# Performance work log

Measured on AMD Instinct MI355X. Metric: run time of the kernel, lower is better.

## Reference

```python
import jax, jax.numpy as jnp
import numpy as np

HEADS = 8
DIM_HEAD = 64
DIM = 512
SCALE = DIM ** -0.5  # NOTE: original scales by dim**-0.5, not dim_head**-0.5


def setup_inputs() -> dict:
    key = jax.random.key(0)
    k1, k2, k3 = jax.random.split(key, 3)
    b, n = 2, 4096
    x = jax.random.normal(k1, (b, n, DIM), dtype=jnp.float32)
    Wqkv = jax.random.normal(k2, (DIM, 3 * HEADS * DIM_HEAD), dtype=jnp.float32) * (DIM ** -0.5)
    Wout = jax.random.normal(k3, (HEADS * DIM_HEAD, DIM), dtype=jnp.float32) * ((HEADS * DIM_HEAD) ** -0.5)
    b_out = jnp.zeros((DIM,), dtype=jnp.float32)
    return {"x": x, "Wqkv": Wqkv, "Wout": Wout, "b_out": b_out}


def reference(x, Wqkv, Wout, b_out):
    b, n, _ = x.shape
    h, d = HEADS, DIM_HEAD
    qkv = x @ Wqkv  # [b, n, 3*h*d]
    q, k, v = jnp.split(qkv, 3, axis=-1)
    to_heads = lambda t: t.reshape(b, n, h, d).transpose(0, 2, 1, 3)  # [b,h,n,d]
    q, k, v = to_heads(q), to_heads(k), to_heads(v)
    half = n // 2
    q_s, q_t = q[:, :, :half], q[:, :, half:]
    k_t = k[:, :, half:]  # k_s is unused in the original module
    v_s, v_t = v[:, :, :half], v[:, :, half:]
    # temporal branch: q_t attends to k_t, reads v_t
    dots_t = jnp.einsum('bhid,bhjd->bhij', q_t, k_t) * SCALE
    # spatial branch: cross-term q_s attends to k_t, reads v_s
    dots_s = jnp.einsum('bhid,bhjd->bhij', q_s, k_t) * SCALE
    attn_s = jax.nn.softmax(dots_s, axis=-1)
    attn_t = jax.nn.softmax(dots_t, axis=-1)
    out_s = jnp.einsum('bhij,bhjd->bhid', attn_s, v_s)
    out_t = jnp.einsum('bhij,bhjd->bhid', attn_t, v_t)
    out = jnp.concatenate([out_s, out_t], axis=2)  # [b,h,n,d]
    out = out.transpose(0, 2, 1, 3).reshape(b, n, h * d)
    return out @ Wout + b_out
```

## Files before the change

### kernel.cpp

```cpp
#include <hip/hip_runtime.h>
#include <hip/hip_bf16.h>

typedef __bf16 bf16;
typedef _Float16 f16;
typedef __bf16 bf16x4 __attribute__((ext_vector_type(4)));
typedef __bf16 bf16x8 __attribute__((ext_vector_type(8)));
typedef _Float16 f16x4 __attribute__((ext_vector_type(4)));
typedef _Float16 f16x8 __attribute__((ext_vector_type(8)));
typedef float floatx4 __attribute__((ext_vector_type(4)));

static __device__ __forceinline__ floatx4 mfma_bf16(bf16x8 a, bf16x8 b, floatx4 c) {
  return __builtin_amdgcn_mfma_f32_16x16x32_bf16(a, b, c, 0, 0, 0);
}
static __device__ __forceinline__ floatx4 mfma_f16k16(f16x4 a, f16x4 b, floatx4 c) {
  return __builtin_amdgcn_mfma_f32_16x16x16f16(a, b, c, 0, 0, 0);
}

static __device__ __forceinline__ bf16x8 cvt8(float4 f0, float4 f1) {
  bf16x8 r;
  r[0] = (bf16)f0.x; r[1] = (bf16)f0.y; r[2] = (bf16)f0.z; r[3] = (bf16)f0.w;
  r[4] = (bf16)f1.x; r[5] = (bf16)f1.y; r[6] = (bf16)f1.z; r[7] = (bf16)f1.w;
  return r;
}

#define HEADS 8
#define DIMH 64
#define DIM 512
#define SEQ 4096
#define HALF 2048
#define BATCH 2
#define MROWS (BATCH * SEQ)
#define ELEMS ((size_t)MROWS * DIM)

#define C2F (0.044194173824159216f * 1.4426950408889634f)

__global__ __launch_bounds__(256)
void transpose_cvt(const float* __restrict__ src, bf16* __restrict__ dst,
                   int K, int N) {
  __shared__ float tile[32][33];
  const int n0 = blockIdx.x * 32, k0 = blockIdx.y * 32;
  const int t = threadIdx.x;
  const int r = t >> 3, c4 = (t & 7) * 4;
  float4 v = *reinterpret_cast<const float4*>(src + (size_t)(k0 + r) * N + n0 + c4);
  tile[r][c4 + 0] = v.x; tile[r][c4 + 1] = v.y;
  tile[r][c4 + 2] = v.z; tile[r][c4 + 3] = v.w;
  __syncthreads();
  bf16x4 o;
#pragma unroll
  for (int i = 0; i < 4; ++i) o[i] = (bf16)tile[c4 + i][r];
  *reinterpret_cast<bf16x4*>(dst + (size_t)(n0 + r) * K + k0 + c4) = o;
}

__global__ __launch_bounds__(256)
void qkv_gemm(const float* __restrict__ X, const bf16* __restrict__ Wt,
              bf16* __restrict__ Qw, bf16* __restrict__ Kw, f16* __restrict__ Vt) {
  __shared__ __align__(16) char smem_raw[36864];
  bf16 (*As)[40] = (bf16(*)[40])smem_raw;
  bf16 (*Bs)[40] = (bf16(*)[40])(smem_raw + 10240);

  const int m0 = blockIdx.x * 128, n0 = blockIdx.y * 128;
  const int t = threadIdx.x;
  const int wave = t >> 6, lane = t & 63, quad = lane >> 4, l16 = lane & 15;
  const int wr = wave >> 1, wc = wave & 1;

  f16 (*Ts)[72] = (f16(*)[72])(smem_raw + wave * 9216);

  floatx4 acc[4][4] = {};

  float4 a0r[2], a1r[2];
  bf16x8 breg[2];
  auto loadk = [&](int k0) {
#pragma unroll
    for (int it = 0; it < 2; ++it) {
      int idx = t + it * 256, row = idx >> 2, c8 = (idx & 3) * 8;
      const float* xp = X + (size_t)(m0 + row) * DIM + k0 + c8;
      a0r[it] = *reinterpret_cast<const float4*>(xp);
      a1r[it] = *reinterpret_cast<const float4*>(xp + 4);
      breg[it] = *reinterpret_cast<const bf16x8*>(Wt + (size_t)(n0 + row) * DIM + k0 + c8);
    }
  };

  loadk(0);
  for (int k0 = 0; k0 < DIM; k0 += 32) {
    __syncthreads();
#pragma unroll
    for (int it = 0; it < 2; ++it) {
      int idx = t + it * 256, row = idx >> 2, c8 = (idx & 3) * 8;
      *reinterpret_cast<bf16x8*>(&As[row][c8]) = cvt8(a0r[it], a1r[it]);
      *reinterpret_cast<bf16x8*>(&Bs[row][c8]) = breg[it];
    }
    __syncthreads();
    int nk = k0 + 32; if (nk >= DIM) nk = 0;
    loadk(nk);

    bf16x8 af[4], bfr[4];
#pragma unroll
    for (int mi = 0; mi < 4; ++mi)
      af[mi] = *reinterpret_cast<const bf16x8*>(&As[wr * 64 + mi * 16 + l16][quad * 8]);
#pragma unroll
    for (int ni = 0; ni < 4; ++ni)
      bfr[ni] = *reinterpret_cast<const bf16x8*>(&Bs[wc * 64 + ni * 16 + l16][quad * 8]);
#pragma unroll
    for (int mi = 0; mi < 4; ++mi)
#pragma unroll
      for (int ni = 0; ni < 4; ++ni)
        acc[mi][ni] = mfma_bf16(af[mi], bfr[ni], acc[mi][ni]);
  }

  if (n0 < 1024) {
#pragma unroll
    for (int mi = 0; mi < 4; ++mi)
#pragma unroll
      for (int ni = 0; ni < 4; ++ni)
#pragma unroll
        for (int r = 0; r < 4; ++r) {
          int row = m0 + wr * 64 + mi * 16 + quad * 4 + r;
          int col = n0 + wc * 64 + ni * 16 + l16;
          int which = col >> 9, cc = col & 511;
          int head = cc >> 6, dim = cc & 63;
          int bb = row >> 12, nn = row & 4095;
          float val = acc[mi][ni][r];
          if (which == 0) val *= C2F;
          bf16* dst = which ? Kw : Qw;
          dst[(((size_t)(bb * HEADS + head)) * SEQ + nn) * DIMH + dim] = (bf16)val;
        }
  } else {
    __syncthreads();
    int head = (n0 + wc * 64 - 1024) >> 6;
#pragma unroll
    for (int mi = 0; mi < 4; ++mi)
#pragma unroll
      for (int ni = 0; ni < 4; ++ni) {
        f16x4 pv;
#pragma unroll
        for (int r = 0; r < 4; ++r) pv[r] = (f16)acc[mi][ni][r];
        *reinterpret_cast<f16x4*>(&Ts[ni * 16 + l16][mi * 16 + quad * 4]) = pv;
      }
    int bb = m0 >> 12, nnb = (m0 + wr * 64) & 4095;
    size_t base = ((size_t)(bb * HEADS + head)) * DIMH;
#pragma unroll
    for (int it = 0; it < 8; ++it) {
      int idx = lane + it * 64;
      int d = idx >> 3, ns = (idx & 7) * 8;
      *reinterpret_cast<f16x8*>(Vt + (base + d) * SEQ + nnb + ns) =
          *reinterpret_cast<const f16x8*>(&Ts[d][ns]);
    }
  }
}

__global__ __launch_bounds__(256, 4)
void attn_kernel(const bf16* __restrict__ Q, const bf16* __restrict__ K,
                 const f16* __restrict__ Vt, bf16* __restrict__ Ow) {
  const int qt = blockIdx.x, h = blockIdx.y, bb = blockIdx.z;
  const int t = threadIdx.x;
  const int lane = t & 63, quad = lane >> 4, l16 = lane & 15;
  const int wave = t >> 6;

  __shared__ bf16 Ks[64][72];
  __shared__ f16 VsT[64][72];

  const size_t hb = ((size_t)(bb * HEADS + h)) * SEQ * DIMH;
  const int vbase = (qt < 32) ? 0 : HALF;
  const int q0 = qt * 64 + wave * 16;

  bf16x8 qa[2];
#pragma unroll
  for (int kc = 0; kc < 2; ++kc)
    qa[kc] = *reinterpret_cast<const bf16x8*>(
        Q + hb + (size_t)(q0 + l16) * DIMH + kc * 32 + quad * 8);

  floatx4 o_acc[4] = {};
  float l_acc = 0.f;

  bf16x8 kreg[2];
  f16x8 vreg[2];
  auto loadc = [&](int kc0) {
#pragma unroll
    for (int it = 0; it < 2; ++it) {
      int idx = t + it * 256, row = idx >> 3, g8 = (idx & 7) * 8;
      kreg[it] = *reinterpret_cast<const bf16x8*>(
          K + hb + (size_t)(HALF + kc0 + row) * DIMH + g8);
      vreg[it] = *reinterpret_cast<const f16x8*>(
          Vt + hb + (size_t)row * SEQ + vbase + kc0 + g8);
    }
  };

  loadc(0);
  for (int kc0 = 0; kc0 < HALF; kc0 += 64) {
    __syncthreads();
#pragma unroll
    for (int it = 0; it < 2; ++it) {
      int idx = t + it * 256, row = idx >> 3, g8 = (idx & 7) * 8;
      *reinterpret_cast<bf16x8*>(&Ks[row][g8]) = kreg[it];
      *reinterpret_cast<f16x8*>(&VsT[row][g8]) = vreg[it];
    }
    __syncthreads();
    int nxt = kc0 + 64; if (nxt >= HALF) nxt = 0;
    loadc(nxt);

#pragma unroll
    for (int kt = 0; kt < 4; ++kt) {
      bf16x8 ka0 = *reinterpret_cast<const bf16x8*>(&Ks[kt * 16 + l16][quad * 8]);
      bf16x8 ka1 = *reinterpret_cast<const bf16x8*>(&Ks[kt * 16 + l16][32 + quad * 8]);
      floatx4 st = {0.f, 0.f, 0.f, 0.f};
      st = mfma_bf16(ka0, qa[0], st);
      st = mfma_bf16(ka1, qa[1], st);
      f16x4 pb;
#pragma unroll
      for (int r = 0; r < 4; ++r) {
        float p = __builtin_amdgcn_exp2f(st[r]);
        l_acc += p;
        pb[r] = (f16)p;
      }
#pragma unroll
      for (int dsub = 0; dsub < 4; ++dsub) {
        f16x4 va = *reinterpret_cast<const f16x4*>(
            &VsT[dsub * 16 + l16][kt * 16 + quad * 4]);
        o_acc[dsub] = mfma_f16k16(va, pb, o_acc[dsub]);
      }
    }
  }

  float v = l_acc;
  v += __shfl_xor(v, 16);
  v += __shfl_xor(v, 32);
  float inv = 1.0f / v;

  int n = q0 + l16;
  size_t rowbase = ((size_t)(bb * SEQ + n)) * DIM + h * DIMH;
#pragma unroll
  for (int dsub = 0; dsub < 4; ++dsub) {
    bf16x4 ov;
#pragma unroll
    for (int r = 0; r < 4; ++r) ov[r] = (bf16)(o_acc[dsub][r] * inv);
    *reinterpret_cast<bf16x4*>(Ow + rowbase + dsub * 16 + quad * 4) = ov;
  }
}

__global__ __launch_bounds__(256)
void out_gemm(const bf16* __restrict__ A, const bf16* __restrict__ Wt,
              const float* __restrict__ bias, float* __restrict__ out) {
  constexpr int Kd = DIM;
  __shared__ bf16 As[64][40];
  __shared__ bf16 Bs[64][40];

  const int m0 = blockIdx.x * 64, n0 = blockIdx.y * 64;
  const int t = threadIdx.x;
  const int wave = t >> 6, lane = t & 63, quad = lane >> 4, l16 = lane & 15;
  const int m_off = (wave >> 1) * 32, n_off = (wave & 1) * 32;

  floatx4 acc[2][2] = {};
  const int srow = t >> 2, scol = (t & 3) * 8;

  bf16x8 areg, breg;
  auto loadk = [&](int k0) {
    areg = *reinterpret_cast<const bf16x8*>(A + (size_t)(m0 + srow) * Kd + k0 + scol);
    breg = *reinterpret_cast<const bf16x8*>(Wt + (size_t)(n0 + srow) * Kd + k0 + scol);
  };

  loadk(0);
  for (int k0 = 0; k0 < Kd; k0 += 32) {
    __syncthreads();
    *reinterpret_cast<bf16x8*>(&As[srow][scol]) = areg;
    *reinterpret_cast<bf16x8*>(&Bs[srow][scol]) = breg;
    __syncthreads();
    int nk = k0 + 32; if (nk >= Kd) nk = 0;
    loadk(nk);

    bf16x8 a0 = *reinterpret_cast<const bf16x8*>(&As[m_off + l16][quad * 8]);
    bf16x8 a1 = *reinterpret_cast<const bf16x8*>(&As[m_off + 16 + l16][quad * 8]);
    bf16x8 b0 = *reinterpret_cast<const bf16x8*>(&Bs[n_off + l16][quad * 8]);
    bf16x8 b1 = *reinterpret_cast<const bf16x8*>(&Bs[n_off + 16 + l16][quad * 8]);
    acc[0][0] = mfma_bf16(a0, b0, acc[0][0]);
    acc[0][1] = mfma_bf16(a0, b1, acc[0][1]);
    acc[1][0] = mfma_bf16(a1, b0, acc[1][0]);
    acc[1][1] = mfma_bf16(a1, b1, acc[1][1]);
  }

#pragma unroll
  for (int mi = 0; mi < 2; ++mi)
#pragma unroll
    for (int ni = 0; ni < 2; ++ni)
#pragma unroll
      for (int r = 0; r < 4; ++r) {
        int row = m0 + m_off + mi * 16 + quad * 4 + r;
        int col = n0 + n_off + ni * 16 + l16;
        out[(size_t)row * DIM + col] = acc[mi][ni][r] + bias[col];
      }
}

extern "C" void kernel_launch(void* const* d_in, const int* in_sizes, int n_in,
                              void* d_out, int out_size, void* d_ws, size_t ws_size,
                              hipStream_t stream) {
  const float* x = (const float*)d_in[0];
  const float* wqkv = (const float*)d_in[1];
  const float* wout = (const float*)d_in[2];
  const float* bout = (const float*)d_in[3];
  float* out = (float*)d_out;

  bf16* Qw = (bf16*)d_ws;
  bf16* Kw = Qw + ELEMS;
  f16* Vt = (f16*)(Kw + ELEMS);
  bf16* Ow = (bf16*)(Vt + ELEMS);
  bf16* WtQKV = Ow + ELEMS;
  bf16* WtOUT = WtQKV + (size_t)1536 * 512;

  transpose_cvt<<<dim3(1536 / 32, DIM / 32), 256, 0, stream>>>(wqkv, WtQKV, DIM, 1536);
  transpose_cvt<<<dim3(DIM / 32, DIM / 32), 256, 0, stream>>>(wout, WtOUT, DIM, DIM);
  qkv_gemm<<<dim3(MROWS / 128, 1536 / 128), 256, 0, stream>>>(x, WtQKV, Qw, Kw, Vt);
  attn_kernel<<<dim3(SEQ / 64, HEADS, BATCH), 256, 0, stream>>>(Qw, Kw, Vt, Ow);
  out_gemm<<<dim3(MROWS / 64, DIM / 64), 256, 0, stream>>>(Ow, WtOUT, bout, out);
}
```

Baseline: 170.5 us.

## Split attention over key halves, widen query tiles, use K32 f16 MFMA, pre-convert X

The attention kernel now processes 128 queries per block (two 16-row tiles per wave) so each K/V tile in shared memory is reused twice. It also splits the key range into two parts across the grid, writing unnormalized f16 partial outputs and row sums. The out_gemm merges the two partials and normalizes while staging A. PV now uses the 16x16x32 f16 MFMA with a permuted K row layout, and X is converted to bf16 in a separate pass before the QKV GEMM. The cost is extra global traffic for two partial outputs plus an extra conversion kernel, and f16 partial accumulators carry some overflow/precision risk.

```diff
diff --git a/kernel.cpp b/kernel.cpp
--- a/kernel.cpp
+++ b/kernel.cpp
@@ -12,8 +12,8 @@
 static __device__ __forceinline__ floatx4 mfma_bf16(bf16x8 a, bf16x8 b, floatx4 c) {
   return __builtin_amdgcn_mfma_f32_16x16x32_bf16(a, b, c, 0, 0, 0);
 }
-static __device__ __forceinline__ floatx4 mfma_f16k16(f16x4 a, f16x4 b, floatx4 c) {
-  return __builtin_amdgcn_mfma_f32_16x16x16f16(a, b, c, 0, 0, 0);
+static __device__ __forceinline__ floatx4 mfma_f16k32(f16x8 a, f16x8 b, floatx4 c) {
+  return __builtin_amdgcn_mfma_f32_16x16x32_f16(a, b, c, 0, 0, 0);
 }
 
 static __device__ __forceinline__ bf16x8 cvt8(float4 f0, float4 f1) {
@@ -33,6 +33,14 @@
 #define ELEMS ((size_t)MROWS * DIM)
 
 #define C2F (0.044194173824159216f * 1.4426950408889634f)
+
+__global__ __launch_bounds__(256)
+void xcvt(const float* __restrict__ X, bf16* __restrict__ Xb) {
+  size_t i = ((size_t)blockIdx.x * 256 + threadIdx.x) * 8;
+  float4 f0 = *reinterpret_cast<const float4*>(X + i);
+  float4 f1 = *reinterpret_cast<const float4*>(X + i + 4);
+  *reinterpret_cast<bf16x8*>(Xb + i) = cvt8(f0, f1);
+}
 
 __global__ __launch_bounds__(256)
 void transpose_cvt(const float* __restrict__ src, bf16* __restrict__ dst,
@@ -52,7 +60,7 @@
 }
 
 __global__ __launch_bounds__(256)
-void qkv_gemm(const float* __restrict__ X, const bf16* __restrict__ Wt,
+void qkv_gemm(const bf16* __restrict__ Xb, const bf16* __restrict__ Wt,
               bf16* __restrict__ Qw, bf16* __restrict__ Kw, f16* __restrict__ Vt) {
   __shared__ __align__(16) char smem_raw[36864];
   bf16 (*As)[40] = (bf16(*)[40])smem_raw;
@@ -67,15 +75,12 @@
 
   floatx4 acc[4][4] = {};
 
-  float4 a0r[2], a1r[2];
-  bf16x8 breg[2];
+  bf16x8 areg[2], breg[2];
   auto loadk = [&](int k0) {
 #pragma unroll
     for (int it = 0; it < 2; ++it) {
       int idx = t + it * 256, row = idx >> 2, c8 = (idx & 3) * 8;
-      const float* xp = X + (size_t)(m0 + row) * DIM + k0 + c8;
-      a0r[it] = *reinterpret_cast<const float4*>(xp);
-      a1r[it] = *reinterpret_cast<const float4*>(xp + 4);
+      areg[it] = *reinterpret_cast<const bf16x8*>(Xb + (size_t)(m0 + row) * DIM + k0 + c8);
       breg[it] = *reinterpret_cast<const bf16x8*>(Wt + (size_t)(n0 + row) * DIM + k0 + c8);
     }
   };
@@ -86,7 +91,7 @@
 #pragma unroll
     for (int it = 0; it < 2; ++it) {
       int idx = t + it * 256, row = idx >> 2, c8 = (idx & 3) * 8;
-      *reinterpret_cast<bf16x8*>(&As[row][c8]) = cvt8(a0r[it], a1r[it]);
+      *reinterpret_cast<bf16x8*>(&As[row][c8]) = areg[it];
       *reinterpret_cast<bf16x8*>(&Bs[row][c8]) = breg[it];
     }
     __syncthreads();
@@ -150,96 +155,135 @@
 
 __global__ __launch_bounds__(256, 4)
 void attn_kernel(const bf16* __restrict__ Q, const bf16* __restrict__ K,
-                 const f16* __restrict__ Vt, bf16* __restrict__ Ow) {
-  const int qt = blockIdx.x, h = blockIdx.y, bb = blockIdx.z;
+                 const f16* __restrict__ Vt, f16* __restrict__ Opart,
+                 float* __restrict__ Lpart) {
+  const int qt = blockIdx.x;
+  const int h = blockIdx.y;
+  const int bb = blockIdx.z >> 1, part = blockIdx.z & 1;
   const int t = threadIdx.x;
-  const int lane = t & 63, quad = lane >> 4, l16 = lane & 15;
-  const int wave = t >> 6;
+  const int wave = t >> 6, lane = t & 63, quad = lane >> 4, l16 = lane & 15;
 
   __shared__ bf16 Ks[64][72];
   __shared__ f16 VsT[64][72];
 
   const size_t hb = ((size_t)(bb * HEADS + h)) * SEQ * DIMH;
-  const int vbase = (qt < 32) ? 0 : HALF;
-  const int q0 = qt * 64 + wave * 16;
-
-  bf16x8 qa[2];
-#pragma unroll
-  for (int kc = 0; kc < 2; ++kc)
-    qa[kc] = *reinterpret_cast<const bf16x8*>(
-        Q + hb + (size_t)(q0 + l16) * DIMH + kc * 32 + quad * 8);
-
-  floatx4 o_acc[4] = {};
-  float l_acc = 0.f;
+  const int vhalf = (qt < 16) ? 0 : HALF;
+  const int kstart = HALF + part * 1024;
+  const int vstart = vhalf + part * 1024;
+  const int q0 = qt * 128 + wave * 32;
+
+  bf16x8 qa[2][2];
+#pragma unroll
+  for (int mt = 0; mt < 2; ++mt)
+#pragma unroll
+    for (int kc = 0; kc < 2; ++kc)
+      qa[mt][kc] = *reinterpret_cast<const bf16x8*>(
+          Q + hb + (size_t)(q0 + mt * 16 + l16) * DIMH + kc * 32 + quad * 8);
+
+  floatx4 o_acc[2][4] = {};
+  float l_acc[2] = {0.f, 0.f};
+
+  int srow[2], sdst[2], g8s;
+  {
+    int r0 = t >> 3;  g8s = (t & 7) * 8;
+#pragma unroll
+    for (int it = 0; it < 2; ++it) {
+      int row = r0 + it * 32;
+      int g32 = row >> 5, w = row & 31, q = w >> 3, j = w & 7;
+      int m = (j < 4) ? (4 * q + j) : (16 + 4 * q + (j - 4));
+      srow[it] = row;
+      sdst[it] = 32 * g32 + m;
+    }
+  }
 
   bf16x8 kreg[2];
   f16x8 vreg[2];
   auto loadc = [&](int kc0) {
 #pragma unroll
     for (int it = 0; it < 2; ++it) {
-      int idx = t + it * 256, row = idx >> 3, g8 = (idx & 7) * 8;
       kreg[it] = *reinterpret_cast<const bf16x8*>(
-          K + hb + (size_t)(HALF + kc0 + row) * DIMH + g8);
+          K + hb + (size_t)(kstart + kc0 + srow[it]) * DIMH + g8s);
       vreg[it] = *reinterpret_cast<const f16x8*>(
-          Vt + hb + (size_t)row * SEQ + vbase + kc0 + g8);
+          Vt + hb + (size_t)srow[it] * SEQ + vstart + kc0 + g8s);
     }
   };
 
   loadc(0);
-  for (int kc0 = 0; kc0 < HALF; kc0 += 64) {
-    __syncthreads();
-#pragma unroll
-    for (int it = 0; it < 2; ++it) {
-      int idx = t + it * 256, row = idx >> 3, g8 = (idx & 7) * 8;
-      *reinterpret_cast<bf16x8*>(&Ks[row][g8]) = kreg[it];
-      *reinterpret_cast<f16x8*>(&VsT[row][g8]) = vreg[it];
-    }
-    __syncthreads();
-    int nxt = kc0 + 64; if (nxt >= HALF) nxt = 0;
+  for (int kc0 = 0; kc0 < 1024; kc0 += 64) {
+    __syncthreads();
+#pragma unroll
+    for (int it = 0; it < 2; ++it) {
+      *reinterpret_cast<bf16x8*>(&Ks[sdst[it]][g8s]) = kreg[it];
+      *reinterpret_cast<f16x8*>(&VsT[srow[it]][g8s]) = vreg[it];
+    }
+    __syncthreads();
+    int nxt = kc0 + 64; if (nxt >= 1024) nxt = 0;
     loadc(nxt);
 
 #pragma unroll
-    for (int kt = 0; kt < 4; ++kt) {
-      bf16x8 ka0 = *reinterpret_cast<const bf16x8*>(&Ks[kt * 16 + l16][quad * 8]);
-      bf16x8 ka1 = *reinterpret_cast<const bf16x8*>(&Ks[kt * 16 + l16][32 + quad * 8]);
-      floatx4 st = {0.f, 0.f, 0.f, 0.f};
-      st = mfma_bf16(ka0, qa[0], st);
-      st = mfma_bf16(ka1, qa[1], st);
-      f16x4 pb;
-#pragma unroll
-      for (int r = 0; r < 4; ++r) {
-        float p = __builtin_amdgcn_exp2f(st[r]);
-        l_acc += p;
-        pb[r] = (f16)p;
+    for (int g = 0; g < 2; ++g) {
+      bf16x8 kaA0 = *reinterpret_cast<const bf16x8*>(&Ks[g * 32 + l16][quad * 8]);
+      bf16x8 kaA1 = *reinterpret_cast<const bf16x8*>(&Ks[g * 32 + l16][32 + quad * 8]);
+      bf16x8 kaB0 = *reinterpret_cast<const bf16x8*>(&Ks[g * 32 + 16 + l16][quad * 8]);
+      bf16x8 kaB1 = *reinterpret_cast<const bf16x8*>(&Ks[g * 32 + 16 + l16][32 + quad * 8]);
+
+      f16x8 pbm[2];
+#pragma unroll
+      for (int mt = 0; mt < 2; ++mt) {
+        floatx4 stA = {0.f, 0.f, 0.f, 0.f}, stB = {0.f, 0.f, 0.f, 0.f};
+        stA = mfma_bf16(kaA0, qa[mt][0], stA);
+        stA = mfma_bf16(kaA1, qa[mt][1], stA);
+        stB = mfma_bf16(kaB0, qa[mt][0], stB);
+        stB = mfma_bf16(kaB1, qa[mt][1], stB);
+        float ls = l_acc[mt];
+        f16x8 pb;
+#pragma unroll
+        for (int r = 0; r < 4; ++r) {
+          float pA = __builtin_amdgcn_exp2f(stA[r]);
+          float pB = __builtin_amdgcn_exp2f(stB[r]);
+          ls += pA + pB;
+          pb[r] = (f16)pA;
+          pb[4 + r] = (f16)pB;
+        }
+        l_acc[mt] = ls;
+        pbm[mt] = pb;
       }
+
 #pragma unroll
       for (int dsub = 0; dsub < 4; ++dsub) {
-        f16x4 va = *reinterpret_cast<const f16x4*>(
-            &VsT[dsub * 16 + l16][kt * 16 + quad * 4]);
-        o_acc[dsub] = mfma_f16k16(va, pb, o_acc[dsub]);
+        f16x8 va = *reinterpret_cast<const f16x8*>(
+            &VsT[dsub * 16 + l16][g * 32 + quad * 8]);
+        o_acc[0][dsub] = mfma_f16k32(va, pbm[0], o_acc[0][dsub]);
+        o_acc[1][dsub] = mfma_f16k32(va, pbm[1], o_acc[1][dsub]);
       }
     }
   }
 
-  float v = l_acc;
-  v += __shfl_xor(v, 16);
-  v += __shfl_xor(v, 32);
-  float inv = 1.0f / v;
-
-  int n = q0 + l16;
-  size_t rowbase = ((size_t)(bb * SEQ + n)) * DIM + h * DIMH;
-#pragma unroll
-  for (int dsub = 0; dsub < 4; ++dsub) {
-    bf16x4 ov;
-#pragma unroll
-    for (int r = 0; r < 4; ++r) ov[r] = (bf16)(o_acc[dsub][r] * inv);
-    *reinterpret_cast<bf16x4*>(Ow + rowbase + dsub * 16 + quad * 4) = ov;
+  f16* Op = Opart + (size_t)part * ELEMS;
+  float* Lp = Lpart + (size_t)part * MROWS * HEADS;
+#pragma unroll
+  for (int mt = 0; mt < 2; ++mt) {
+    float v = l_acc[mt];
+    v += __shfl_xor(v, 16);
+    v += __shfl_xor(v, 32);
+    int n = q0 + mt * 16 + l16;
+    size_t rowidx = (size_t)(bb * SEQ + n);
+    if (quad == 0) Lp[rowidx * HEADS + h] = v;
+    size_t rowbase = rowidx * DIM + h * DIMH;
+#pragma unroll
+    for (int dsub = 0; dsub < 4; ++dsub) {
+      f16x4 ov;
+#pragma unroll
+      for (int r = 0; r < 4; ++r) ov[r] = (f16)o_acc[mt][dsub][r];
+      *reinterpret_cast<f16x4*>(Op + rowbase + dsub * 16 + quad * 4) = ov;
+    }
   }
 }
 
 __global__ __launch_bounds__(256)
-void out_gemm(const bf16* __restrict__ A, const bf16* __restrict__ Wt,
-              const float* __restrict__ bias, float* __restrict__ out) {
+void out_gemm(const f16* __restrict__ Opart, const float* __restrict__ Lpart,
+              const bf16* __restrict__ Wt, const float* __restrict__ bias,
+              float* __restrict__ out) {
   constexpr int Kd = DIM;
   __shared__ bf16 As[64][40];
   __shared__ bf16 Bs[64][40];
@@ -249,20 +293,38 @@
   const int wave = t >> 6, lane = t & 63, quad = lane >> 4, l16 = lane & 15;
   const int m_off = (wave >> 1) * 32, n_off = (wave & 1) * 32;
 
+  const f16* O1 = Opart;
+  const f16* O2 = Opart + ELEMS;
+  const float* L1 = Lpart;
+  const float* L2 = Lpart + (size_t)MROWS * HEADS;
+
   floatx4 acc[2][2] = {};
   const int srow = t >> 2, scol = (t & 3) * 8;
 
-  bf16x8 areg, breg;
+  f16x8 o1r, o2r;
+  float lr;
+  bf16x8 breg;
   auto loadk = [&](int k0) {
-    areg = *reinterpret_cast<const bf16x8*>(A + (size_t)(m0 + srow) * Kd + k0 + scol);
+    int kcol = k0 + scol, hh = kcol >> 6;
+    size_t arow = (size_t)(m0 + srow);
+    o1r = *reinterpret_cast<const f16x8*>(O1 + arow * DIM + kcol);
+    o2r = *reinterpret_cast<const f16x8*>(O2 + arow * DIM + kcol);
+    lr = L1[arow * HEADS + hh] + L2[arow * HEADS + hh];
     breg = *reinterpret_cast<const bf16x8*>(Wt + (size_t)(n0 + srow) * Kd + k0 + scol);
   };
 
   loadk(0);
   for (int k0 = 0; k0 < Kd; k0 += 32) {
     __syncthreads();
-    *reinterpret_cast<bf16x8*>(&As[srow][scol]) = areg;
-    *reinterpret_cast<bf16x8*>(&Bs[srow][scol]) = breg;
+    {
+      float inv = 1.0f / lr;
+      bf16x8 a;
+#pragma unroll
+      for (int j = 0; j < 8; ++j)
+        a[j] = (bf16)(((float)o1r[j] + (float)o2r[j]) * inv);
+      *reinterpret_cast<bf16x8*>(&As[srow][scol]) = a;
+      *reinterpret_cast<bf16x8*>(&Bs[srow][scol]) = breg;
+    }
     __syncthreads();
     int nk = k0 + 32; if (nk >= Kd) nk = 0;
     loadk(nk);
@@ -301,13 +363,16 @@
   bf16* Qw = (bf16*)d_ws;
   bf16* Kw = Qw + ELEMS;
   f16* Vt = (f16*)(Kw + ELEMS);
-  bf16* Ow = (bf16*)(Vt + ELEMS);
-  bf16* WtQKV = Ow + ELEMS;
+  f16* Opart = Vt + ELEMS;
+  bf16* Xb = (bf16*)(Opart + 2 * ELEMS);
+  bf16* WtQKV = Xb + ELEMS;
   bf16* WtOUT = WtQKV + (size_t)1536 * 512;
-
+  float* Lpart = (float*)(WtOUT + (size_t)512 * 512);
+
+  xcvt<<<ELEMS / 2048, 256, 0, stream>>>(x, Xb);
   transpose_cvt<<<dim3(1536 / 32, DIM / 32), 256, 0, stream>>>(wqkv, WtQKV, DIM, 1536);
   transpose_cvt<<<dim3(DIM / 32, DIM / 32), 256, 0, stream>>>(wout, WtOUT, DIM, DIM);
-  qkv_gemm<<<dim3(MROWS / 128, 1536 / 128), 256, 0, stream>>>(x, WtQKV, Qw, Kw, Vt);
-  attn_kernel<<<dim3(SEQ / 64, HEADS, BATCH), 256, 0, stream>>>(Qw, Kw, Vt, Ow);
-  out_gemm<<<dim3(MROWS / 64, DIM / 64), 256, 0, stream>>>(Ow, WtOUT, bout, out);
-}
+  qkv_gemm<<<dim3(MROWS / 128, 1536 / 128), 256, 0, stream>>>(Xb, WtQKV, Qw, Kw, Vt);
+  attn_kernel<<<dim3(SEQ / 128, HEADS, BATCH * 2), 256, 0, stream>>>(Qw, Kw, Vt, Opart, Lpart);
+  out_gemm<<<dim3(MROWS / 64, DIM / 64), 256, 0, stream>>>(Opart, Lpart, WtOUT, bout, out);
+}
```

Result: faster. 165.1 us (-3.2%).
